# Optimization experiments

Hardware: AMD Instinct MI355X
Metric: run time of the kernel (lower is better)

## Reference

```python
import jax, jax.numpy as jnp
import numpy as np

B, C, H, W = 16, 256, 64, 64
LDCE, CDCE = 100, 128


def _conv(x, w, groups=1):
    # x: NCHW, w: OIHW, stride 1, SAME padding (matches pad=1 for 3x3, pad=0 for 1x1)
    return jax.lax.conv_general_dilated(x, w, (1, 1), 'SAME',
                                        feature_group_count=groups,
                                        dimension_numbers=('NCHW', 'OIHW', 'NCHW'))


def _bn(x, g, b, eps=1e-5):
    # training-mode BatchNorm2d: biased batch stats over (N,H,W)
    m = jnp.mean(x, axis=(0, 2, 3), keepdims=True)
    v = jnp.var(x, axis=(0, 2, 3), keepdims=True)
    return g[None, :, None, None] * (x - m) * jax.lax.rsqrt(v + eps) + b[None, :, None, None]


def _silu(z):
    return z * jax.nn.sigmoid(z)


def setup_inputs() -> dict:
    key = jax.random.key(0)
    ks = jax.random.split(key, 18)
    f32 = jnp.float32
    s = 0.05
    d = {}
    d['x'] = jax.random.normal(ks[0], (B, C, H, W), f32)
    d['dce_output'] = jax.random.normal(ks[1], (B, LDCE, CDCE), f32)
    # DCE projection Linear(dce_dim -> out_feat)
    d['w_dce'] = jax.random.normal(ks[2], (C, CDCE), f32) * s
    d['b_dce'] = jax.random.normal(ks[3], (C,), f32) * s
    # per-channel 3x3 convs, stacked as a depthwise kernel (C,1,3,3)
    d['w_ch'] = jax.random.normal(ks[4], (C, 1, 3, 3), f32) * s
    # shrink / expand MLP
    d['w_shrink'] = jax.random.normal(ks[5], (C // 2, C), f32) * s
    d['b_shrink'] = jax.random.normal(ks[6], (C // 2,), f32) * s
    d['w_expand'] = jax.random.normal(ks[7], (C, C // 2), f32) * s
    d['b_expand'] = jax.random.normal(ks[8], (C,), f32) * s
    # ResBlock backbone: conv3x3 -> BN -> SiLU -> conv1x1 -> BN
    d['w_conv1'] = jax.random.normal(ks[9], (C, C, 3, 3), f32) * s
    d['g_bn1'] = jnp.ones((C,), f32)
    d['be_bn1'] = jnp.zeros((C,), f32)
    d['w_conv2'] = jax.random.normal(ks[10], (C, C, 1, 1), f32) * s
    d['g_bn2'] = jnp.ones((C,), f32)
    d['be_bn2'] = jnp.zeros((C,), f32)
    # shortcut: conv1x1 -> BN
    d['w_sc'] = jax.random.normal(ks[11], (C, C, 1, 1), f32) * s
    d['g_bns'] = jnp.ones((C,), f32)
    d['be_bns'] = jnp.zeros((C,), f32)
    return d


def reference(x, dce_output, w_dce, b_dce, w_ch, w_shrink, b_shrink,
              w_expand, b_expand, w_conv1, g_bn1, be_bn1, w_conv2, g_bn2,
              be_bn2, w_sc, g_bns, be_bns):
    C2 = w_dce.shape[0]
    # 1. AdaptiveAvgPool1d(1) over sequence, then Linear: (B, C2)
    dce_pooled = jnp.mean(dce_output, axis=1)            # (B, CDCE)
    dce_proj = dce_pooled @ w_dce.T + b_dce              # (B, C2)
    # 2. per-channel Conv2d(1,1,3) + global avg pool == depthwise conv + mean
    conv_out = _conv(x, w_ch, groups=C2)                 # (B, C2, H, W)
    spatial_proj = jnp.mean(conv_out, axis=(2, 3))       # (B, C2)
    # 3-5. modulation gate
    m = dce_proj * spatial_proj
    h = jax.nn.relu(m @ w_shrink.T + b_shrink)
    mod = jax.nn.sigmoid(h @ w_expand.T + b_expand)      # (B, C2)
    # 6. channel-wise modulation
    xm = x * mod[:, :, None, None]
    # 7. ResBlock
    bb = _silu(_bn(_conv(xm, w_conv1), g_bn1, be_bn1))
    bb = _bn(_conv(bb, w_conv2), g_bn2, be_bn2)
    sc = _bn(_conv(xm, w_sc), g_bns, be_bns)
    return _silu(bb + sc)
```

## Files before the change

kernel.cpp:

```cpp
#include <hip/hip_runtime.h>

typedef unsigned short u16;
typedef unsigned int   u32;
typedef __attribute__((ext_vector_type(8))) __bf16 bf16x8;
typedef __attribute__((ext_vector_type(4))) float  f32x4;

#define HW 4096
#define NPOS 65536
#define CH 256
#define MT 512
#define NMT 256

__device__ __forceinline__ u16 f2bf(float f){
  u32 u = __float_as_uint(f);
  u += 0x7FFFu + ((u >> 16) & 1u);
  return (u16)(u >> 16);
}
__device__ __forceinline__ float bflo(u32 p){ return __uint_as_float(p << 16); }
__device__ __forceinline__ float bfhi(u32 p){ return __uint_as_float(p & 0xFFFF0000u); }

#define GLL16(g, l) __builtin_amdgcn_global_load_lds( \
    (__attribute__((address_space(1))) void*)(g), \
    (__attribute__((address_space(3))) void*)(l), 16, 0, 0)

#define VM8() asm volatile("s_waitcnt vmcnt(8)" ::: "memory")
#define VM4() asm volatile("s_waitcnt vmcnt(4)" ::: "memory")
#define VM0() asm volatile("s_waitcnt vmcnt(0)" ::: "memory")
#define BARX() do { __builtin_amdgcn_s_barrier(); __builtin_amdgcn_sched_barrier(0); } while(0)

__global__ __launch_bounds__(256) void k_statsx(const float* __restrict__ x, float* __restrict__ stats){
  int bc = blockIdx.x; int tid = threadIdx.x;
  const float* xp = x + (size_t)bc * HW;
  float S=0.f, r0=0.f, r1=0.f, c0=0.f, c1=0.f;
  #pragma unroll
  for (int k=0;k<4;k++){
    int i4 = tid + k*256;
    float4 v = ((const float4*)xp)[i4];
    int pos = i4*4; int h = pos>>6; int wb = pos&63;
    float sv = v.x+v.y+v.z+v.w;
    S += sv;
    if (h==0)  r0 += sv;
    if (h==63) r1 += sv;
    if (wb==0)  c0 += v.x;
    if (wb==60) c1 += v.w;
  }
  __shared__ float red[4][5];
  #pragma unroll
  for (int off=32; off>0; off>>=1){
    S  += __shfl_down(S, off);
    r0 += __shfl_down(r0, off);
    r1 += __shfl_down(r1, off);
    c0 += __shfl_down(c0, off);
    c1 += __shfl_down(c1, off);
  }
  if ((tid & 63) == 0){
    int w = tid >> 6;
    red[w][0]=S; red[w][1]=r0; red[w][2]=r1; red[w][3]=c0; red[w][4]=c1;
  }
  __syncthreads();
  if (tid == 0){
    float* o = stats + (size_t)bc * 9;
    for (int j=0;j<5;j++) o[j] = red[0][j]+red[1][j]+red[2][j]+red[3][j];
    o[5] = xp[0];
    o[6] = xp[63];
    o[7] = xp[4032];
    o[8] = xp[4095];
  }
}

__global__ __launch_bounds__(256) void k_gate(const float* __restrict__ dce,
    const float* __restrict__ stats, const float* __restrict__ wch,
    const float* __restrict__ w_dce, const float* __restrict__ b_dce,
    const float* __restrict__ w_sh, const float* __restrict__ b_sh,
    const float* __restrict__ w_ex, const float* __restrict__ b_ex,
    float* __restrict__ modb){
  int b = blockIdx.x, tid = threadIdx.x;
  __shared__ float pl[128];
  __shared__ float mbuf[256];
  __shared__ float hbuf[128];
  __shared__ float ptmp[256];
  {
    int k = tid & 127, half = tid >> 7;
    const float* p = dce + (size_t)b*12800 + half*50*128 + k;
    float s = 0.f;
    #pragma unroll 5
    for (int l=0;l<50;l++) s += p[l*128];
    ptmp[tid] = s;
  }
  __syncthreads();
  if (tid < 128) pl[tid] = (ptmp[tid] + ptmp[tid+128]) * 0.01f;
  __syncthreads();
  {
    int c = tid;
    const float* st = stats + (size_t)(b*256+c)*9;
    float S=st[0], r0=st[1], r1=st[2], cc0=st[3], cc1=st[4];
    float x00=st[5], x0W=st[6], xH0=st[7], xHW=st[8];
    float acc = 0.f;
    #pragma unroll
    for (int t=0;t<9;t++){
      int dh = t/3 - 1, dw = t%3 - 1;
      float R = (dh==1)? r0 : (dh==-1)? r1 : 0.f;
      float Cc = (dw==1)? cc0 : (dw==-1)? cc1 : 0.f;
      float X = 0.f;
      if (dh==1 && dw==1) X = x00;
      else if (dh==1 && dw==-1) X = x0W;
      else if (dh==-1 && dw==1) X = xH0;
      else if (dh==-1 && dw==-1) X = xHW;
      acc += wch[c*9+t] * (S - R - Cc + X);
    }
    float sp_ = acc * (1.f/4096.f);
    float dp = b_dce[c];
    const float4* wr = (const float4*)(w_dce + c*128);
    #pragma unroll 8
    for (int k4=0;k4<32;k4++){
      float4 w4 = wr[k4];
      dp += w4.x*pl[k4*4] + w4.y*pl[k4*4+1] + w4.z*pl[k4*4+2] + w4.w*pl[k4*4+3];
    }
    mbuf[c] = sp_ * dp;
  }
  __syncthreads();
  if (tid < 128){
    int j = tid;
    float acc = b_sh[j];
    const float4* wr = (const float4*)(w_sh + j*256);
    #pragma unroll 8
    for (int k4=0;k4<64;k4++){
      float4 w4 = wr[k4];
      acc += w4.x*mbuf[k4*4] + w4.y*mbuf[k4*4+1] + w4.z*mbuf[k4*4+2] + w4.w*mbuf[k4*4+3];
    }
    hbuf[j] = fmaxf(acc, 0.f);
  }
  __syncthreads();
  {
    int c = tid;
    float acc = b_ex[c];
    const float4* wr = (const float4*)(w_ex + c*128);
    #pragma unroll 8
    for (int k4=0;k4<32;k4++){
      float4 w4 = wr[k4];
      acc += w4.x*hbuf[k4*4] + w4.y*hbuf[k4*4+1] + w4.z*hbuf[k4*4+2] + w4.w*hbuf[k4*4+3];
    }
    modb[b*256+c] = 1.f/(1.f + __expf(-acc));
  }
}

__global__ __launch_bounds__(256) void k_wprep(const float* __restrict__ w1,
    const float* __restrict__ wsc, const float* __restrict__ w2,
    u16* __restrict__ w1t, u16* __restrict__ wsct, u16* __restrict__ w2t){
  int bx = blockIdx.x, ci = threadIdx.x;
  if (bx < 2304){
    int co = bx / 9, t = bx - co*9;
    w1t[(size_t)co*2304 + t*256 + ci] = f2bf(w1[(size_t)(co*256+ci)*9 + t]);
  } else if (bx < 2560){
    int i = (bx-2304)*256 + ci;
    wsct[i] = f2bf(wsc[i]);
  } else {
    int i = (bx-2560)*256 + ci;
    w2t[i] = f2bf(w2[i]);
  }
}

__global__ __launch_bounds__(256) void k_xm(const float* __restrict__ x, const float* __restrict__ modb,
                                            u16* __restrict__ xm){
  __shared__ __attribute__((aligned(16))) u16 tile[64*266];
  int pt = blockIdx.x, ct = blockIdx.y, tid = threadIdx.x;
  size_t P0 = (size_t)pt * 256;
  int b = pt >> 4;
  int rem = (pt & 15) << 8;
  int C0 = ct << 6;
  {
    int c = tid >> 2, q = tid & 3;
    const float* xp = x + ((size_t)(b*256 + C0 + c))*HW + rem;
    float mv = modb[b*256 + C0 + c];
    #pragma unroll
    for (int k=0;k<16;k++){
      int pos = q*64 + k*4;
      float4 v = *(const float4*)(xp + pos);
      u32 w0 = (u32)f2bf(v.x*mv) | ((u32)f2bf(v.y*mv) << 16);
      u32 w1 = (u32)f2bf(v.z*mv) | ((u32)f2bf(v.w*mv) << 16);
      u32* dst = (u32*)&tile[c*266 + pos];
      dst[0] = w0; dst[1] = w1;
    }
  }
  __syncthreads();
  {
    int g = tid & 7, p0 = tid >> 3;
    #pragma unroll
    for (int k=0;k<8;k++){
      int pos = p0 + k*32;
      u32 v0 = tile[(g*8+0)*266 + pos], v1 = tile[(g*8+1)*266 + pos];
      u32 v2 = tile[(g*8+2)*266 + pos], v3 = tile[(g*8+3)*266 + pos];
      u32 v4 = tile[(g*8+4)*266 + pos], v5 = tile[(g*8+5)*266 + pos];
      u32 v6 = tile[(g*8+6)*266 + pos], v7 = tile[(g*8+7)*266 + pos];
      uint4 pk;
      pk.x = v0 | (v1<<16); pk.y = v2 | (v3<<16);
      pk.z = v4 | (v5<<16); pk.w = v6 | (v7<<16);
      *(uint4*)(xm + (P0+pos)*CH + C0 + g*8) = pk;
    }
  }
}

template<int NTAPS>
__global__ __launch_bounds__(512, 2) void k_gemm8p(const u16* __restrict__ A,
    const u16* __restrict__ Bw, u16* __restrict__ y,
    float* __restrict__ psum, float* __restrict__ psq, const u16* __restrict__ zp){
  constexpr int KTOT = NTAPS*256;
  constexpr int NT = KTOT/32;
  __shared__ __attribute__((aligned(16))) u16 SH[65536];
  int tid = threadIdx.x;
  int lane = tid & 63, wave = tid >> 6;
  int wm = wave >> 2, wn = wave & 3;
  int l15 = lane & 15, quad = lane >> 4;
  int mt = blockIdx.x;
  int P0 = mt*256;

  int rdx   = (((l15>>3)&1)<<4) | (((l15>>2)&1)<<3);
  int kphys = (quad*8) ^ rdx;
  int aoff  = (wm*128 + l15)*32 + kphys;
  int boff  = 32768 + (wn*64 + l15)*32 + kphys;

  int pr = tid >> 2;
  int kb = (tid&3) ^ ((((tid>>5)&1)<<1) | ((tid>>4)&1));
  int k0 = kb*8;
  int pos0 = P0 + pr, pos1 = P0 + 128 + pr;
  int hh0 = (pos0>>6)&63, ww0 = pos0&63;
  int hh1 = (pos1>>6)&63, ww1 = pos1&63;

  f32x4 acc[8][4];
  f32x4 zz = {0.f,0.f,0.f,0.f};
  #pragma unroll
  for (int i=0;i<8;i++)
    #pragma unroll
    for (int j=0;j<4;j++) acc[i][j] = zz;

  auto stageA = [&](int ktn){
    int set = ktn & 3;
    if constexpr (NTAPS == 9){
      int tap = ktn >> 3;
      int t3 = tap/3;
      int dh = t3 - 1, dw = (tap - t3*3) - 1;
      int d = dh*64 + dw;
      int coff = ((ktn & 7)*32) + k0;
      bool ok0 = ((unsigned)(hh0+dh) < 64u) && ((unsigned)(ww0+dw) < 64u);
      bool ok1 = ((unsigned)(hh1+dh) < 64u) && ((unsigned)(ww1+dw) < 64u);
      const u16* s0 = ok0 ? A + (size_t)(pos0 + d)*CH + coff : zp + coff;
      const u16* s1 = ok1 ? A + (size_t)(pos1 + d)*CH + coff : zp + coff;
      GLL16(s0, SH + set*8192 + wave*512);
      GLL16(s1, SH + set*8192 + 4096 + wave*512);
    } else {
      const u16* s0 = A + (size_t)pos0*CH + ktn*32 + k0;
      const u16* s1 = A + (size_t)pos1*CH + ktn*32 + k0;
      GLL16(s0, SH + set*8192 + wave*512);
      GLL16(s1, SH + set*8192 + 4096 + wave*512);
    }
  };
  auto stageB = [&](int ktn){
    int set = ktn & 3;
    const u16* s0 = Bw + (size_t)pr*KTOT + ktn*32 + k0;
    const u16* s1 = Bw + (size_t)(pr+128)*KTOT + ktn*32 + k0;
    GLL16(s0, SH + 32768 + set*8192 + wave*512);
    GLL16(s1, SH + 32768 + set*8192 + 4096 + wave*512);
  };

  stageA(0); stageB(0);
  stageA(1); stageB(1);
  stageA(2); stageB(2);
  VM8();
  BARX();

  for (int w = 0; w < NT; ++w){
    int sb = (w & 3)*8192;
    bf16x8 af[4], bv[4];
    #pragma unroll
    for (int i=0;i<4;i++) af[i] = *(const bf16x8*)&SH[sb + aoff + i*512];
    #pragma unroll
    for (int j=0;j<4;j++) bv[j] = *(const bf16x8*)&SH[sb + boff + j*512];
    if (w+3 < NT) stageA(w+3);
    BARX();
    __builtin_amdgcn_s_setprio(1);
    #pragma unroll
    for (int i=0;i<4;i++)
      #pragma unroll
      for (int j=0;j<4;j++)
        acc[i][j] = __builtin_amdgcn_mfma_f32_16x16x32_bf16(af[i], bv[j], acc[i][j], 0, 0, 0);
    __builtin_amdgcn_s_setprio(0);
    BARX();
    #pragma unroll
    for (int i=0;i<4;i++) af[i] = *(const bf16x8*)&SH[sb + aoff + 2048 + i*512];
    if (w+3 < NT) stageB(w+3);
    if (w < NT-3)      { VM8(); }
    else if (w == NT-3){ VM4(); }
    else if (w == NT-2){ VM0(); }
    BARX();
    __builtin_amdgcn_s_setprio(1);
    #pragma unroll
    for (int i=0;i<4;i++)
      #pragma unroll
      for (int j=0;j<4;j++)
        acc[4+i][j] = __builtin_amdgcn_mfma_f32_16x16x32_bf16(af[i], bv[j], acc[4+i][j], 0, 0, 0);
    __builtin_amdgcn_s_setprio(0);
    BARX();
  }

  #pragma unroll
  for (int i=0;i<8;i++){
    int m = wm*128 + i*16 + quad*4;
    #pragma unroll
    for (int j=0;j<4;j++){
      int n = wn*64 + j*16 + l15;
      size_t base = ((size_t)(P0 + m))*CH + n;
      #pragma unroll
      for (int r=0;r<4;r++)
        y[base + (size_t)r*CH] = f2bf(acc[i][j][r]);
    }
  }
  float* SHf = (float*)SH;
  #pragma unroll
  for (int j=0;j<4;j++){
    float a=0.f, b=0.f;
    #pragma unroll
    for (int i=0;i<8;i++)
      #pragma unroll
      for (int r=0;r<4;r++){ float v = acc[i][j][r]; a += v; b += v*v; }
    a += __shfl_xor(a,16); b += __shfl_xor(b,16);
    a += __shfl_xor(a,32); b += __shfl_xor(b,32);
    if (quad==0){
      int idx = ((wave*4 + j)*16 + l15)*2;
      SHf[idx] = a; SHf[idx+1] = b;
    }
  }
  __syncthreads();
  if (tid < 256){
    int n = tid; int wnn = n>>6; int j = (n>>4)&3; int li = n&15;
    int i0 = (((wnn)*4 + j)*16 + li)*2;
    int i1 = (((4+wnn)*4 + j)*16 + li)*2;
    psum[(size_t)n*NMT + mt] = SHf[i0] + SHf[i1];
    psq [(size_t)n*NMT + mt] = SHf[i0+1] + SHf[i1+1];
  }
}

__global__ __launch_bounds__(64) void k_bnstat(const float* __restrict__ psum, const float* __restrict__ psq,
    const float* __restrict__ g, const float* __restrict__ be,
    float* __restrict__ scale, float* __restrict__ shift){
  int c = blockIdx.x, t = threadIdx.x;
  const float* ps = psum + (size_t)c*NMT;
  const float* pq = psq  + (size_t)c*NMT;
  float s=0.f, q=0.f;
  #pragma unroll
  for (int i=0;i<4;i++){ s += ps[t + i*64]; q += pq[t + i*64]; }
  #pragma unroll
  for (int off=32; off>0; off>>=1){
    s += __shfl_down(s, off);
    q += __shfl_down(q, off);
  }
  if (t == 0){
    float mean = s * (1.f/65536.f);
    float var  = q * (1.f/65536.f) - mean*mean;
    float rstd = rsqrtf(var + 1e-5f);
    float sc = g[c]*rstd;
    scale[c] = sc;
    shift[c] = be[c] - mean*sc;
  }
}

__global__ __launch_bounds__(256) void k_bb(const u16* __restrict__ y1, const float* __restrict__ sc1,
    const float* __restrict__ sh1, u16* __restrict__ bb){
  __shared__ float sc[256], sh[256];
  int tid = threadIdx.x;
  sc[tid] = sc1[tid]; sh[tid] = sh1[tid];
  __syncthreads();
  size_t i = ((size_t)blockIdx.x*256 + tid)*8;
  int c0 = (int)(i & 255);
  uint4 v = *(const uint4*)(y1 + i);
  u32 a[4] = {v.x, v.y, v.z, v.w};
  u32 o[4];
  #pragma unroll
  for (int p=0;p<4;p++){
    float zl = sc[c0+2*p]*bflo(a[p]) + sh[c0+2*p];
    float zh = sc[c0+2*p+1]*bfhi(a[p]) + sh[c0+2*p+1];
    float ol = zl/(1.f+__expf(-zl));
    float oh = zh/(1.f+__expf(-zh));
    o[p] = (u32)f2bf(ol) | ((u32)f2bf(oh) << 16);
  }
  uint4 w; w.x=o[0]; w.y=o[1]; w.z=o[2]; w.w=o[3];
  *(uint4*)(bb + i) = w;
}

__global__ __launch_bounds__(256) void k_final(const u16* __restrict__ y2, const u16* __restrict__ ysc,
    const float* __restrict__ sc2, const float* __restrict__ sh2,
    const float* __restrict__ scs, const float* __restrict__ shs,
    float* __restrict__ out){
  __shared__ __attribute__((aligned(16))) float tile[64*257];
  __shared__ float l2s[64], l2h[64], lss[64], lsh[64];
  int pt = blockIdx.x, ct = blockIdx.y, tid = threadIdx.x;
  int C0 = ct << 6;
  if (tid < 64){ l2s[tid]=sc2[C0+tid]; l2h[tid]=sh2[C0+tid]; lss[tid]=scs[C0+tid]; lsh[tid]=shs[C0+tid]; }
  __syncthreads();
  size_t P0 = (size_t)pt * 256;
  int b = pt >> 4; int rem = (pt & 15) << 8;
  {
    int g = tid & 7, p0 = tid >> 3;
    for (int k=0;k<8;k++){
      int pos = p0 + k*32;
      size_t off = (P0+pos)*CH + C0 + g*8;
      uint4 va = *(const uint4*)(y2 + off);
      uint4 vb = *(const uint4*)(ysc + off);
      u32 aa[4] = {va.x,va.y,va.z,va.w};
      u32 bv[4] = {vb.x,vb.y,vb.z,vb.w};
      #pragma unroll
      for (int p=0;p<4;p++){
        int c = g*8 + 2*p;
        float z0 = l2s[c]*bflo(aa[p]) + l2h[c] + lss[c]*bflo(bv[p]) + lsh[c];
        float z1 = l2s[c+1]*bfhi(aa[p]) + l2h[c+1] + lss[c+1]*bfhi(bv[p]) + lsh[c+1];
        tile[c*257 + pos]     = z0/(1.f+__expf(-z0));
        tile[(c+1)*257 + pos] = z1/(1.f+__expf(-z1));
      }
    }
  }
  __syncthreads();
  {
    int c = tid >> 2, q = tid & 3;
    float* op = out + ((size_t)(b*256 + C0 + c))*HW + rem;
    #pragma unroll
    for (int k=0;k<16;k++){
      int pos = q*64 + k*4;
      float4 v;
      v.x = tile[c*257 + pos];
      v.y = tile[c*257 + pos + 1];
      v.z = tile[c*257 + pos + 2];
      v.w = tile[c*257 + pos + 3];
      *(float4*)(op + pos) = v;
    }
  }
}

extern "C" void kernel_launch(void* const* d_in, const int* in_sizes, int n_in,
                              void* d_out, int out_size, void* d_ws, size_t ws_size,
                              hipStream_t stream){
  const float* x     = (const float*)d_in[0];
  const float* dce   = (const float*)d_in[1];
  const float* w_dce = (const float*)d_in[2];
  const float* b_dce = (const float*)d_in[3];
  const float* w_ch  = (const float*)d_in[4];
  const float* w_sh  = (const float*)d_in[5];
  const float* b_sh  = (const float*)d_in[6];
  const float* w_ex  = (const float*)d_in[7];
  const float* b_ex  = (const float*)d_in[8];
  const float* w_c1  = (const float*)d_in[9];
  const float* g1    = (const float*)d_in[10];
  const float* be1   = (const float*)d_in[11];
  const float* w_c2  = (const float*)d_in[12];
  const float* g2    = (const float*)d_in[13];
  const float* be2   = (const float*)d_in[14];
  const float* w_s   = (const float*)d_in[15];
  const float* gs    = (const float*)d_in[16];
  const float* bes   = (const float*)d_in[17];
  float* out = (float*)d_out;
  char* ws = (char*)d_ws;

  const size_t NB = (size_t)NPOS*CH*2;
  u16* xm  = (u16*)(ws);
  u16* y1  = (u16*)(ws + NB);
  u16* ysc = (u16*)(ws + 2*NB);
  u16* bb  = (u16*)(ws + 3*NB);
  char* p = ws + 4*NB;
  u16* w1t   = (u16*)p; p += (size_t)256*2304*2;
  u16* wsct  = (u16*)p; p += (size_t)256*256*2;
  u16* w2t   = (u16*)p; p += (size_t)256*256*2;
  float* statsx = (float*)p; p += (size_t)16*256*9*4;
  float* modb   = (float*)p; p += (size_t)16*256*4;
  float* p1s = (float*)p; p += (size_t)MT*256*4;
  float* p1q = (float*)p; p += (size_t)MT*256*4;
  float* pss = (float*)p; p += (size_t)MT*256*4;
  float* psqv= (float*)p; p += (size_t)MT*256*4;
  float* p2s = (float*)p; p += (size_t)MT*256*4;
  float* p2q = (float*)p; p += (size_t)MT*256*4;
  float* bn1sc = (float*)p; p += 1024;
  float* bn1sh = (float*)p; p += 1024;
  float* bnssc = (float*)p; p += 1024;
  float* bnssh = (float*)p; p += 1024;
  float* bn2sc = (float*)p; p += 1024;
  float* bn2sh = (float*)p; p += 1024;
  u16* zp = (u16*)p; p += 4096;

  hipMemsetAsync(zp, 0, 4096, stream);
  k_statsx<<<4096, 256, 0, stream>>>(x, statsx);
  k_wprep<<<2816, 256, 0, stream>>>(w_c1, w_s, w_c2, w1t, wsct, w2t);
  k_gate<<<16, 256, 0, stream>>>(dce, statsx, w_ch, w_dce, b_dce, w_sh, b_sh, w_ex, b_ex, modb);
  k_xm<<<dim3(256,4), 256, 0, stream>>>(x, modb, xm);
  k_gemm8p<9><<<256, 512, 0, stream>>>(xm, w1t, y1, p1s, p1q, zp);
  k_bnstat<<<256, 64, 0, stream>>>(p1s, p1q, g1, be1, bn1sc, bn1sh);
  k_bb<<<8192, 256, 0, stream>>>(y1, bn1sc, bn1sh, bb);
  k_gemm8p<1><<<256, 512, 0, stream>>>(xm, wsct, ysc, pss, psqv, zp);
  k_bnstat<<<256, 64, 0, stream>>>(pss, psqv, gs, bes, bnssc, bnssh);
  k_gemm8p<1><<<256, 512, 0, stream>>>(bb, w2t, y1 , p2s, p2q, zp);
  k_bnstat<<<256, 64, 0, stream>>>(p2s, p2q, g2, be2, bn2sc, bn2sh);
  k_final<<<dim3(256,4), 256, 0, stream>>>(y1, ysc, bn2sc, bn2sh, bnssc, bnssh, out);
}
```

Before: 393.3 us.

## Restructure GEMM main loop to 64-wide K tiles with quadrant-split double buffering

The implicit-GEMM conv kernel now uses K-steps of 64 instead of 32, with a new XOR-swizzled LDS layout and a double-buffered scheme that splits A and B tiles into halves. Each K-step is computed as four MFMA quadrants, and global-to-LDS loads of the next tiles are interleaved between them. The goal is fewer barriers and wait points per unit of work and better overlap of loads with MFMA. The cost is more register pressure from holding A and B fragments for both halves, plus a more intricate vmcnt/barrier schedule that could stall or race if miscounted.

```diff
diff --git a/kernel.cpp b/kernel.cpp
--- a/kernel.cpp
+++ b/kernel.cpp
@@ -23,10 +23,29 @@
     (__attribute__((address_space(1))) void*)(g), \
     (__attribute__((address_space(3))) void*)(l), 16, 0, 0)
 
-#define VM8() asm volatile("s_waitcnt vmcnt(8)" ::: "memory")
 #define VM4() asm volatile("s_waitcnt vmcnt(4)" ::: "memory")
 #define VM0() asm volatile("s_waitcnt vmcnt(0)" ::: "memory")
 #define BARX() do { __builtin_amdgcn_s_barrier(); __builtin_amdgcn_sched_barrier(0); } while(0)
+#define SP1() __builtin_amdgcn_s_setprio(1)
+#define SP0() __builtin_amdgcn_s_setprio(0)
+
+#define MMQ(Aa, Bb, IO, JO) \
+  { _Pragma("unroll") for (int fi=0; fi<4; fi++){ \
+      _Pragma("unroll") for (int fj=0; fj<2; fj++){ \
+        acc[(IO)+fi][(JO)+fj] = __builtin_amdgcn_mfma_f32_16x16x32_bf16(Aa[0][fi], Bb[0][fj], acc[(IO)+fi][(JO)+fj], 0,0,0); \
+        acc[(IO)+fi][(JO)+fj] = __builtin_amdgcn_mfma_f32_16x16x32_bf16(Aa[1][fi], Bb[1][fj], acc[(IO)+fi][(JO)+fj], 0,0,0); \
+  } } }
+
+#define RDA(dst, D, QOFF) \
+  { _Pragma("unroll") for (int fi=0; fi<4; fi++){ \
+      dst[0][fi] = *(const bf16x8*)&SH[(D) + aBase + (QOFF) + fi*1024 + kx0]; \
+      dst[1][fi] = *(const bf16x8*)&SH[(D) + aBase + (QOFF) + fi*1024 + kx1]; \
+  } }
+#define RDB(dst, D, JOFF) \
+  { _Pragma("unroll") for (int fj=0; fj<2; fj++){ \
+      dst[0][fj] = *(const bf16x8*)&SH[(D) + bBase + (JOFF) + fj*1024 + kx0]; \
+      dst[1][fj] = *(const bf16x8*)&SH[(D) + bBase + (JOFF) + fj*1024 + kx1]; \
+  } }
 
 __global__ __launch_bounds__(256) void k_statsx(const float* __restrict__ x, float* __restrict__ stats){
   int bc = blockIdx.x; int tid = threadIdx.x;
@@ -205,7 +224,8 @@
     const u16* __restrict__ Bw, u16* __restrict__ y,
     float* __restrict__ psum, float* __restrict__ psq, const u16* __restrict__ zp){
   constexpr int KTOT = NTAPS*256;
-  constexpr int NT = KTOT/32;
+  constexpr int NT = KTOT/64;
+  constexpr int NI = NT/2;
   __shared__ __attribute__((aligned(16))) u16 SH[65536];
   int tid = threadIdx.x;
   int lane = tid & 63, wave = tid >> 6;
@@ -214,17 +234,15 @@
   int mt = blockIdx.x;
   int P0 = mt*256;
 
-  int rdx   = (((l15>>3)&1)<<4) | (((l15>>2)&1)<<3);
-  int kphys = (quad*8) ^ rdx;
-  int aoff  = (wm*128 + l15)*32 + kphys;
-  int boff  = 32768 + (wn*64 + l15)*32 + kphys;
-
-  int pr = tid >> 2;
-  int kb = (tid&3) ^ ((((tid>>5)&1)<<1) | ((tid>>4)&1));
-  int k0 = kb*8;
-  int pos0 = P0 + pr, pos1 = P0 + 128 + pr;
-  int hh0 = (pos0>>6)&63, ww0 = pos0&63;
-  int hh1 = (pos1>>6)&63, ww1 = pos1&63;
+  int s3  = l15 & 7;
+  int kx0 = ((quad)     ^ s3) * 8;
+  int kx1 = ((4 | quad) ^ s3) * 8;
+  int aBase = wm*8192 + l15*64;
+  int bBase = 32768 + (wn>>1)*8192 + (wn&1)*4096 + l15*64;
+
+  int r0  = tid >> 3;
+  int c0  = (tid & 7) ^ (r0 & 7);
+  int csrc = c0 * 8;
 
   f32x4 acc[8][4];
   f32x4 zz = {0.f,0.f,0.f,0.f};
@@ -233,72 +251,87 @@
     #pragma unroll
     for (int j=0;j<4;j++) acc[i][j] = zz;
 
-  auto stageA = [&](int ktn){
-    int set = ktn & 3;
+  auto stageA = [&](int t, int ah){
+    int base = (t&1)*16384 + ah*8192;
     if constexpr (NTAPS == 9){
-      int tap = ktn >> 3;
+      int tap = t >> 2, koff = (t & 3) << 6;
       int t3 = tap/3;
       int dh = t3 - 1, dw = (tap - t3*3) - 1;
       int d = dh*64 + dw;
-      int coff = ((ktn & 7)*32) + k0;
-      bool ok0 = ((unsigned)(hh0+dh) < 64u) && ((unsigned)(ww0+dw) < 64u);
-      bool ok1 = ((unsigned)(hh1+dh) < 64u) && ((unsigned)(ww1+dw) < 64u);
-      const u16* s0 = ok0 ? A + (size_t)(pos0 + d)*CH + coff : zp + coff;
-      const u16* s1 = ok1 ? A + (size_t)(pos1 + d)*CH + coff : zp + coff;
-      GLL16(s0, SH + set*8192 + wave*512);
-      GLL16(s1, SH + set*8192 + 4096 + wave*512);
+      #pragma unroll
+      for (int L=0; L<2; L++){
+        int pos = P0 + ah*128 + (L<<6) + r0;
+        int h = (pos>>6)&63, w = pos&63;
+        bool ok = ((unsigned)(h+dh) < 64u) && ((unsigned)(w+dw) < 64u);
+        const u16* s = ok ? A + (size_t)(pos + d)*CH + koff + csrc : zp + csrc;
+        GLL16(s, SH + base + L*4096 + tid*8);
+      }
     } else {
-      const u16* s0 = A + (size_t)pos0*CH + ktn*32 + k0;
-      const u16* s1 = A + (size_t)pos1*CH + ktn*32 + k0;
-      GLL16(s0, SH + set*8192 + wave*512);
-      GLL16(s1, SH + set*8192 + 4096 + wave*512);
+      #pragma unroll
+      for (int L=0; L<2; L++){
+        int pos = P0 + ah*128 + (L<<6) + r0;
+        const u16* s = A + (size_t)pos*CH + t*64 + csrc;
+        GLL16(s, SH + base + L*4096 + tid*8);
+      }
     }
   };
-  auto stageB = [&](int ktn){
-    int set = ktn & 3;
-    const u16* s0 = Bw + (size_t)pr*KTOT + ktn*32 + k0;
-    const u16* s1 = Bw + (size_t)(pr+128)*KTOT + ktn*32 + k0;
-    GLL16(s0, SH + 32768 + set*8192 + wave*512);
-    GLL16(s1, SH + 32768 + set*8192 + 4096 + wave*512);
+  auto stageB = [&](int t, int bh){
+    int base = 32768 + (t&1)*16384 + bh*8192;
+    #pragma unroll
+    for (int L=0; L<2; L++){
+      int co = bh*128 + (L<<6) + r0;
+      const u16* s = Bw + (size_t)co*KTOT + t*64 + csrc;
+      GLL16(s, SH + base + L*4096 + tid*8);
+    }
   };
 
-  stageA(0); stageB(0);
-  stageA(1); stageB(1);
-  stageA(2); stageB(2);
-  VM8();
+  stageA(0,0); stageA(0,1); stageB(0,0); stageB(0,1);
+  stageA(1,0); stageA(1,1);
+  VM4();
   BARX();
 
-  for (int w = 0; w < NT; ++w){
-    int sb = (w & 3)*8192;
-    bf16x8 af[4], bv[4];
-    #pragma unroll
-    for (int i=0;i<4;i++) af[i] = *(const bf16x8*)&SH[sb + aoff + i*512];
-    #pragma unroll
-    for (int j=0;j<4;j++) bv[j] = *(const bf16x8*)&SH[sb + boff + j*512];
-    if (w+3 < NT) stageA(w+3);
-    BARX();
-    __builtin_amdgcn_s_setprio(1);
-    #pragma unroll
-    for (int i=0;i<4;i++)
-      #pragma unroll
-      for (int j=0;j<4;j++)
-        acc[i][j] = __builtin_amdgcn_mfma_f32_16x16x32_bf16(af[i], bv[j], acc[i][j], 0, 0, 0);
-    __builtin_amdgcn_s_setprio(0);
-    BARX();
-    #pragma unroll
-    for (int i=0;i<4;i++) af[i] = *(const bf16x8*)&SH[sb + aoff + 2048 + i*512];
-    if (w+3 < NT) stageB(w+3);
-    if (w < NT-3)      { VM8(); }
-    else if (w == NT-3){ VM4(); }
-    else if (w == NT-2){ VM0(); }
-    BARX();
-    __builtin_amdgcn_s_setprio(1);
-    #pragma unroll
-    for (int i=0;i<4;i++)
-      #pragma unroll
-      for (int j=0;j<4;j++)
-        acc[4+i][j] = __builtin_amdgcn_mfma_f32_16x16x32_bf16(af[i], bv[j], acc[4+i][j], 0, 0, 0);
-    __builtin_amdgcn_s_setprio(0);
+  bf16x8 aLo[2][4], aHi[2][4], bLo[2][2], bHi[2][2];
+
+  for (int n=0; n<NI; ++n){
+    const int t1 = 2*n+1;
+    const bool pre = (n+1 < NI);
+    RDA(aLo, 0, 0); RDB(bLo, 0, 0);
+    stageB(t1, 0);
+    BARX();
+    SP1(); MMQ(aLo, bLo, 0, 0); SP0();
+    BARX();
+    RDA(aHi, 0, 4096);
+    stageB(t1, 1);
+    BARX();
+    SP1(); MMQ(aHi, bLo, 4, 0); SP0();
+    BARX();
+    RDB(bHi, 0, 2048);
+    if (pre) stageA(t1+1, 0);
+    BARX();
+    SP1(); MMQ(aHi, bHi, 4, 2); SP0();
+    BARX();
+    if (pre){ stageA(t1+1, 1); VM4(); } else { VM0(); }
+    BARX();
+    SP1(); MMQ(aLo, bHi, 0, 2); SP0();
+    BARX();
+    RDA(aLo, 16384, 0); RDB(bLo, 16384, 0);
+    if (pre) stageB(t1+1, 0);
+    BARX();
+    SP1(); MMQ(aLo, bLo, 0, 0); SP0();
+    BARX();
+    RDA(aHi, 16384, 4096);
+    if (pre) stageB(t1+1, 1);
+    BARX();
+    SP1(); MMQ(aHi, bLo, 4, 0); SP0();
+    BARX();
+    RDB(bHi, 16384, 2048);
+    if (pre) stageA(t1+2, 0);
+    BARX();
+    SP1(); MMQ(aHi, bHi, 4, 2); SP0();
+    BARX();
+    if (pre){ stageA(t1+2, 1); VM4(); }
+    BARX();
+    SP1(); MMQ(aLo, bHi, 0, 2); SP0();
     BARX();
   }
 
```

Result: no change. 389.8 us (-0.9%).
